# Kernel tuning notes

Hardware: AMD Instinct MI355X
Metric: run time of the kernel (lower is better)

## Reference

```python
import jax, jax.numpy as jnp
from jax import lax
import numpy as np

N, F_IN, D_MODEL = 8192, 128, 256
D_INNER, D_STATE, D_CONV, DT_RANK = 512, 16, 4, 16  # expand=2, d_state=16, d_conv=4, dt_rank=ceil(256/16)
BN_EPS = 1e-5


def setup_inputs() -> dict:
    key = jax.random.key(0)
    ks = jax.random.split(key, 12)
    rn = lambda k, s, sc: jax.random.normal(k, s, jnp.float32) * sc
    x = rn(ks[0], (N, F_IN), 1.0)
    # normalized dense adjacency (row sums ~1)
    adj = jax.random.uniform(ks[1], (N, N), jnp.float32) * (2.0 / N)
    w_gcn = rn(ks[2], (F_IN, D_MODEL), 1.0 / np.sqrt(F_IN))
    b_gcn = rn(ks[3], (D_MODEL,), 0.02)
    bn_gamma = jnp.ones((D_MODEL,), jnp.float32)
    bn_beta = jnp.zeros((D_MODEL,), jnp.float32)
    w_in = rn(ks[4], (2 * D_INNER, D_MODEL), 1.0 / np.sqrt(D_MODEL))
    conv_w = rn(ks[5], (D_INNER, D_CONV), 1.0 / np.sqrt(D_CONV))
    conv_b = rn(ks[6], (D_INNER,), 0.02)
    w_xproj = rn(ks[7], (DT_RANK + 2 * D_STATE, D_INNER), 1.0 / np.sqrt(D_INNER))
    w_dt = rn(ks[8], (D_INNER, DT_RANK), 1.0 / np.sqrt(DT_RANK))
    b_dt = rn(ks[9], (D_INNER,), 0.1)
    A_log = jnp.log(jnp.broadcast_to(jnp.arange(1, D_STATE + 1, dtype=jnp.float32), (D_INNER, D_STATE)))
    D_skip = jnp.ones((D_INNER,), jnp.float32)
    w_out = rn(ks[10], (D_MODEL, D_INNER), 1.0 / np.sqrt(D_INNER))
    return dict(x=x, adj=adj, w_gcn=w_gcn, b_gcn=b_gcn, bn_gamma=bn_gamma, bn_beta=bn_beta,
                w_in=w_in, conv_w=conv_w, conv_b=conv_b, w_xproj=w_xproj, w_dt=w_dt,
                b_dt=b_dt, A_log=A_log, D_skip=D_skip, w_out=w_out)


def _forward(x, adj, w_gcn, b_gcn, bn_gamma, bn_beta, w_in, conv_w, conv_b,
             w_xproj, w_dt, b_dt, A_log, D_skip, w_out):
    # --- GCN layer: adj @ (x @ W) + b ---
    h = adj @ (x @ w_gcn) + b_gcn            # (N, D_MODEL)
    h = jax.nn.relu(h)
    # dropout: eval mode -> identity
    # --- BatchNorm1d (batch statistics, biased var, as torch training norm) ---
    mean = jnp.mean(h, axis=0)
    var = jnp.var(h, axis=0)
    h = (h - mean) * lax.rsqrt(var + BN_EPS) * bn_gamma + bn_beta  # (N, D_MODEL)

    # --- Mamba block, batch=1, seq_len=N ---
    xz = h @ w_in.T                          # (N, 2*D_INNER)
    xm, z = jnp.split(xz, 2, axis=-1)        # (N, D_INNER) each

    # causal depthwise conv1d (kernel D_CONV) + SiLU
    xp = jnp.pad(xm, ((D_CONV - 1, 0), (0, 0)))
    xc = conv_b + sum(xp[i:i + N] * conv_w[:, i] for i in range(D_CONV))  # (N, D_INNER)
    xc = jax.nn.silu(xc)

    # input-dependent SSM parameters
    x_dbl = xc @ w_xproj.T                   # (N, DT_RANK + 2*D_STATE)
    dt_r = x_dbl[:, :DT_RANK]
    B = x_dbl[:, DT_RANK:DT_RANK + D_STATE]  # (N, D_STATE)
    C = x_dbl[:, DT_RANK + D_STATE:]         # (N, D_STATE)
    dt = jax.nn.softplus(dt_r @ w_dt.T + b_dt)  # (N, D_INNER)

    A = -jnp.exp(A_log)                      # (D_INNER, D_STATE)
    deltaA = jnp.exp(dt[:, :, None] * A[None])                 # (N, D_INNER, D_STATE)
    deltaBu = dt[:, :, None] * B[:, None, :] * xc[:, :, None]  # (N, D_INNER, D_STATE)

    def step(hs, inp):
        dA, dBu, c = inp
        hs = dA * hs + dBu                   # (D_INNER, D_STATE)
        return hs, hs @ c                    # emit (D_INNER,)

    h0 = jnp.zeros((D_INNER, D_STATE), xc.dtype)
    _, ys = lax.scan(step, h0, (deltaA, deltaBu, C))  # ys: (N, D_INNER)

    y = ys + D_skip * xc
    y = y * jax.nn.silu(z)
    out_m = y @ w_out.T                      # (N, D_MODEL)
    return out_m + h                         # residual


def reference(x, adj, w_gcn, b_gcn, bn_gamma, bn_beta, w_in, conv_w, conv_b,
              w_xproj, w_dt, b_dt, A_log, D_skip, w_out):
    return _forward(x, adj, w_gcn, b_gcn, bn_gamma, bn_beta, w_in, conv_w, conv_b,
                    w_xproj, w_dt, b_dt, A_log, D_skip, w_out)
```

## Files before the change

### kernel.cpp

```cpp
#include <hip/hip_runtime.h>
#include <stdint.h>

#define NN   8192
#define FIN  128
#define DM   256
#define DI   512
#define DST  16
#define NC   256
#define CL   32

typedef short bf16x8 __attribute__((ext_vector_type(8)));
typedef float f32x4 __attribute__((ext_vector_type(4)));
union FragU { unsigned u[4]; uint4 u4; bf16x8 v; };

__device__ __forceinline__ unsigned short f2bf(float x){
  unsigned u = __float_as_uint(x);
  return (unsigned short)((u + 0x7FFFu + ((u >> 16) & 1u)) >> 16);
}
__device__ __forceinline__ unsigned pack2(float a, float b){
  return (unsigned)f2bf(a) | ((unsigned)f2bf(b) << 16);
}
__device__ __forceinline__ unsigned pack2rn(float a, float b){
  unsigned ua = __float_as_uint(a) + 0x8000u;
  unsigned ub = __float_as_uint(b) + 0x8000u;
  return __builtin_amdgcn_perm(ub, ua, 0x07060302u);
}
__device__ __forceinline__ float bf2f(unsigned short u){
  return __uint_as_float(((unsigned)u) << 16);
}
__device__ __forceinline__ float sigmoidf_(float x){ return 1.f / (1.f + __expf(-x)); }
__device__ __forceinline__ f32x4 zero4(){ f32x4 z; z[0]=0.f; z[1]=0.f; z[2]=0.f; z[3]=0.f; return z; }

#define ASYNC16(g, l) __builtin_amdgcn_global_load_lds( \
    (const __attribute__((address_space(1))) void*)(g), \
    (__attribute__((address_space(3))) void*)(l), 16, 0, 0)
#define WAITVM8  asm volatile("s_waitcnt vmcnt(8)" ::: "memory")
#define WAITVM4  asm volatile("s_waitcnt vmcnt(4)" ::: "memory")
#define WAITVM3  asm volatile("s_waitcnt vmcnt(3)" ::: "memory")
#define WAITVM0  asm volatile("s_waitcnt vmcnt(0)" ::: "memory")
#define WAITLGKM0 asm volatile("s_waitcnt lgkmcnt(0)" ::: "memory")
#define BARRIER  asm volatile("s_barrier" ::: "memory")

constexpr size_t OFF_XWT   = 0;
constexpr size_t OFF_HB    = OFF_XWT   + (size_t)DM*NN*2;
constexpr size_t OFF_HBNB  = OFF_HB    + (size_t)NN*DM*2;
constexpr size_t OFF_WINB  = OFF_HBNB  + (size_t)NN*DM*2;
constexpr size_t OFF_WXPB  = OFF_WINB  + (size_t)1024*256*2;
constexpr size_t OFF_WOUTB = OFF_WXPB  + (size_t)48*512*2;
constexpr size_t OFF_XMB   = OFF_WOUTB + (size_t)256*512*2;
constexpr size_t OFF_ZB    = OFF_XMB   + (size_t)NN*DI*2;
constexpr size_t OFF_XC    = OFF_ZB    + (size_t)NN*DI*2;
constexpr size_t OFF_XCB   = OFF_XC    + (size_t)NN*DI*4;
constexpr size_t OFF_XDBL  = OFF_XCB   + (size_t)NN*DI*2;
constexpr size_t OFF_DT    = OFF_XDBL  + (size_t)NN*48*4;
constexpr size_t OFF_PF    = OFF_DT    + (size_t)NN*DI*4;
constexpr size_t OFF_CY    = OFF_PF    + (size_t)NC*DI*DST*8;
constexpr size_t OFF_YB    = OFF_CY    + (size_t)NC*DI*DST*4;
constexpr size_t OFF_BNS   = OFF_YB    + (size_t)NN*DI*2;
constexpr size_t OFF_BNS2  = OFF_BNS   + 256*4;
constexpr size_t WS_NEED   = OFF_BNS2  + 256*4;
constexpr size_t OFF_HP    = OFF_PF;

__global__ __launch_bounds__(256) void prep_kernel(
    const float* __restrict__ w_in, const float* __restrict__ w_xp, const float* __restrict__ w_out,
    unsigned short* __restrict__ o_in, unsigned short* __restrict__ o_xp, unsigned short* __restrict__ o_out)
{
  int i = blockIdx.x * 256 + threadIdx.x;
  if (i < 1024*256) o_in[i]  = f2bf(w_in[i]);
  if (i < 48*512)   o_xp[i]  = f2bf(w_xp[i]);
  if (i < 256*512)  o_out[i] = f2bf(w_out[i]);
}

__global__ __launch_bounds__(256) void gemm1_kernel(
    const float* __restrict__ x, const float* __restrict__ w, unsigned short* __restrict__ xwT)
{
  __shared__ float xs[16*128];
  const int t = threadIdx.x;
  const int m0 = blockIdx.x * 16;
  {
    int r = t >> 4, c0 = (t & 15) * 8;
    const float* src = x + (size_t)(m0 + r)*FIN + c0;
    *(float4*)&xs[r*128 + c0]     = *(const float4*)src;
    *(float4*)&xs[r*128 + c0 + 4] = *(const float4*)(src + 4);
  }
  __syncthreads();
  const int n = t;
  float acc[16];
  #pragma unroll
  for (int m = 0; m < 16; ++m) acc[m] = 0.f;
  for (int k = 0; k < 128; k += 4){
    float w0 = w[(size_t)k*DM + n];
    float w1 = w[(size_t)(k+1)*DM + n];
    float w2 = w[(size_t)(k+2)*DM + n];
    float w3 = w[(size_t)(k+3)*DM + n];
    #pragma unroll
    for (int m = 0; m < 16; ++m){
      float4 xv = *(const float4*)&xs[m*128 + k];
      acc[m] = fmaf(xv.x, w0, acc[m]);
      acc[m] = fmaf(xv.y, w1, acc[m]);
      acc[m] = fmaf(xv.z, w2, acc[m]);
      acc[m] = fmaf(xv.w, w3, acc[m]);
    }
  }
  unsigned outp[8];
  #pragma unroll
  for (int m = 0; m < 8; ++m) outp[m] = pack2(acc[2*m], acc[2*m+1]);
  unsigned short* dst = xwT + (size_t)n*NN + m0;
  ((uint4*)dst)[0] = *(uint4*)&outp[0];
  ((uint4*)dst)[1] = *(uint4*)&outp[4];
}

__global__ __launch_bounds__(512, 1) void gemm2_kernel(
    const float* __restrict__ adj, const unsigned short* __restrict__ xwT,
    float* __restrict__ hp)
{
  extern __shared__ char lds[];
  const int t = threadIdx.x;
  const int wave = t >> 6, lane = t & 63, r = lane & 15, q = lane >> 4;
  const int mt = (int)blockIdx.x >> 2, ks = (int)blockIdx.x & 3;
  const int m0 = mt * 128;
  const int kb = ks * 2048;
  const int wm = wave & 1, wn = wave >> 1;

  const int arow = t >> 3, ag = t & 7;
  const float* asrcA = adj + (size_t)(m0 + arow)*NN + kb + ((ag ^ (arow & 7)) << 2);
  const float* asrcB = asrcA + (size_t)64*NN;
  const int bnl = t >> 2, bg = t & 3;
  const unsigned short* bsrcA = xwT + (size_t)bnl*NN + kb + ((bg ^ ((bnl >> 1) & 3)) << 3);
  const unsigned short* bsrcB = bsrcA + (size_t)128*NN;
  const int dA0 = t*16, dA1 = 8192 + t*16, dB0 = 16384 + t*16, dB1 = 24576 + t*16;

  f32x4 acc[4][4];
  #pragma unroll
  for (int mi = 0; mi < 4; ++mi)
    #pragma unroll
    for (int ni = 0; ni < 4; ++ni) acc[mi][ni] = zero4();

  #pragma unroll
  for (int s = 0; s < 3; ++s){
    char* L = lds + s*32768;
    ASYNC16(asrcA + s*32, L + dA0);
    ASYNC16(asrcB + s*32, L + dA1);
    ASYNC16(bsrcA + s*32, L + dB0);
    ASYNC16(bsrcB + s*32, L + dB1);
  }

  int aoff[4][2], boff[4];
  #pragma unroll
  for (int mi = 0; mi < 4; ++mi){
    int row = wm*64 + mi*16 + r;
    aoff[mi][0] = row*32 + (((2*q)   ^ (row & 7)) << 2);
    aoff[mi][1] = row*32 + (((2*q+1) ^ (row & 7)) << 2);
  }
  #pragma unroll
  for (int ni = 0; ni < 4; ++ni){
    int nl = wn*64 + ni*16 + r;
    boff[ni] = nl*4 + (q ^ ((nl >> 1) & 3));
  }

  int rb = 0;
  for (int k = 0; k < 64; ++k){
    if (k < 62) { WAITVM8; } else if (k == 62) { WAITVM4; } else { WAITVM0; }
    BARRIER;
    char* Lb = lds + rb*32768;
    const float* Af = (const float*)Lb;
    const uint4* Bf = (const uint4*)(Lb + 16384);
    float4 pa[4][2];
    FragU fb[4];
    #pragma unroll
    for (int mi = 0; mi < 4; ++mi){
      pa[mi][0] = *(const float4*)(Af + aoff[mi][0]);
      pa[mi][1] = *(const float4*)(Af + aoff[mi][1]);
    }
    #pragma unroll
    for (int ni = 0; ni < 4; ++ni) fb[ni].u4 = Bf[boff[ni]];
    WAITLGKM0;
    BARRIER;
    if (k < 61){
      int ko = (k + 3) * 32;
      ASYNC16(asrcA + ko, Lb + dA0);
      ASYNC16(asrcB + ko, Lb + dA1);
      ASYNC16(bsrcA + ko, Lb + dB0);
      ASYNC16(bsrcB + ko, Lb + dB1);
    }
    FragU fa[4];
    #pragma unroll
    for (int mi = 0; mi < 4; ++mi){
      fa[mi].u[0] = pack2rn(pa[mi][0].x, pa[mi][0].y);
      fa[mi].u[1] = pack2rn(pa[mi][0].z, pa[mi][0].w);
      fa[mi].u[2] = pack2rn(pa[mi][1].x, pa[mi][1].y);
      fa[mi].u[3] = pack2rn(pa[mi][1].z, pa[mi][1].w);
    }
    #pragma unroll
    for (int mi = 0; mi < 4; ++mi)
      #pragma unroll
      for (int ni = 0; ni < 4; ++ni)
        acc[mi][ni] = __builtin_amdgcn_mfma_f32_16x16x32_bf16(fa[mi].v, fb[ni].v, acc[mi][ni], 0, 0, 0);
    rb = (rb == 2) ? 0 : rb + 1;
  }

  float* hpo = hp + (size_t)ks * ((size_t)NN * DM);
  #pragma unroll
  for (int mi = 0; mi < 4; ++mi)
    #pragma unroll
    for (int ni = 0; ni < 4; ++ni){
      const int n = wn*64 + ni*16 + r;
      #pragma unroll
      for (int jr = 0; jr < 4; ++jr){
        const int m = m0 + wm*64 + mi*16 + q*4 + jr;
        hpo[(size_t)m*DM + n] = acc[mi][ni][jr];
      }
    }
}

__global__ __launch_bounds__(256) void hred_kernel(
    const float* __restrict__ hp, const float* __restrict__ b_gcn,
    unsigned short* __restrict__ hb, float* __restrict__ bns, float* __restrict__ bns2)
{
  const size_t NND = (size_t)NN * DM;
  const int c = threadIdx.x;
  const int m0 = blockIdx.x * 32;
  const float bias = b_gcn[c];
  float s1 = 0.f, s2 = 0.f;
  #pragma unroll 8
  for (int rr = 0; rr < 32; ++rr){
    size_t idx = (size_t)(m0 + rr)*DM + c;
    float v = hp[idx] + hp[NND + idx] + hp[2*NND + idx] + hp[3*NND + idx] + bias;
    v = fmaxf(v, 0.f);
    hb[idx] = f2bf(v);
    s1 += v; s2 += v*v;
  }
  atomicAdd(bns + c, s1);
  atomicAdd(bns2 + c, s2);
}

__global__ __launch_bounds__(256) void bnapply_kernel(
    const unsigned short* __restrict__ hb, const float* __restrict__ s1, const float* __restrict__ s2,
    const float* __restrict__ gamma, const float* __restrict__ beta,
    unsigned short* __restrict__ hbnb)
{
  int base = (blockIdx.x*256 + threadIdx.x) * 2;
  int c0 = base & (DM - 1);
  ushort2 hv = *(const ushort2*)(hb + base);
  float mA = s1[c0] * (1.f/NN),   mB = s1[c0+1] * (1.f/NN);
  float vA = s2[c0] * (1.f/NN) - mA*mA, vB = s2[c0+1] * (1.f/NN) - mB*mB;
  float iA = rsqrtf(vA + 1e-5f), iB = rsqrtf(vB + 1e-5f);
  float a = (bf2f(hv.x) - mA)*iA*gamma[c0]   + beta[c0];
  float b = (bf2f(hv.y) - mB)*iB*gamma[c0+1] + beta[c0+1];
  ushort2 o; o.x = f2bf(a); o.y = f2bf(b);
  *(ushort2*)(hbnb + base) = o;
}

__global__ __launch_bounds__(256) void gemm3_kernel(
    const unsigned short* __restrict__ Ab, const unsigned short* __restrict__ Wb,
    unsigned short* __restrict__ xmb, unsigned short* __restrict__ zb)
{
  __shared__ uint4 alds[2048];
  const int t = threadIdx.x;
  const int wave = t >> 6, lane = t & 63, r = lane & 15, q = lane >> 4;
  const int mb = ((int)blockIdx.x & 127) * 64;
  const int nb = ((int)blockIdx.x >> 7) * 128;
  const int wm = wave & 1, wn = wave >> 1;

  #pragma unroll
  for (int j = 0; j < 8; ++j){
    int si = j*256 + t;
    int row = si >> 5, dg = si & 31;
    int sg = dg ^ (row & 31);
    ASYNC16(Ab + (size_t)(mb + row)*DM + sg*8, (char*)alds + si*16);
  }
  __syncthreads();

  f32x4 acc[2][4];
  #pragma unroll
  for (int mi = 0; mi < 2; ++mi)
    #pragma unroll
    for (int ni = 0; ni < 4; ++ni) acc[mi][ni] = zero4();

  const unsigned short* bp[4];
  #pragma unroll
  for (int ni = 0; ni < 4; ++ni)
    bp[ni] = Wb + (size_t)(nb + wn*64 + ni*16 + r)*DM + q*8;
  FragU fb[4];
  #pragma unroll
  for (int ni = 0; ni < 4; ++ni) fb[ni].u4 = *(const uint4*)bp[ni];

  #pragma unroll
  for (int it = 0; it < 8; ++it){
    FragU fbn[4];
    if (it < 7){
      #pragma unroll
      for (int ni = 0; ni < 4; ++ni) fbn[ni].u4 = *(const uint4*)(bp[ni] + (it+1)*32);
    }
    FragU fa[2];
    #pragma unroll
    for (int mi = 0; mi < 2; ++mi){
      int row = wm*32 + mi*16 + r;
      int g = it*4 + q;
      fa[mi].u4 = alds[row*32 + (g ^ (row & 31))];
    }
    #pragma unroll
    for (int mi = 0; mi < 2; ++mi)
      #pragma unroll
      for (int ni = 0; ni < 4; ++ni)
        acc[mi][ni] = __builtin_amdgcn_mfma_f32_16x16x32_bf16(fa[mi].v, fb[ni].v, acc[mi][ni], 0, 0, 0);
    if (it < 7){
      #pragma unroll
      for (int ni = 0; ni < 4; ++ni) fb[ni] = fbn[ni];
    }
  }
  #pragma unroll
  for (int mi = 0; mi < 2; ++mi)
    #pragma unroll
    for (int ni = 0; ni < 4; ++ni){
      int nc = nb + wn*64 + ni*16 + r;
      unsigned short* dst = (nc < 512) ? (xmb + nc) : (zb + (nc - 512));
      #pragma unroll
      for (int jr = 0; jr < 4; ++jr){
        int m = mb + wm*32 + mi*16 + q*4 + jr;
        dst[(size_t)m*DI] = f2bf(acc[mi][ni][jr]);
      }
    }
}

__global__ __launch_bounds__(256) void conv_kernel(
    const unsigned short* __restrict__ xmb, const float* __restrict__ conv_w, const float* __restrict__ conv_b,
    float* __restrict__ xc, unsigned short* __restrict__ xcb)
{
  const int d0 = threadIdx.x * 2;
  const int n0 = blockIdx.x * 32;
  float4 wa = *(const float4*)(conv_w + (size_t)d0*4);
  float4 wb = *(const float4*)(conv_w + (size_t)d0*4 + 4);
  float2 bias = *(const float2*)(conv_b + d0);
  float x0a=0.f,x1a=0.f,x2a=0.f, x0b=0.f,x1b=0.f,x2b=0.f;
  #pragma unroll
  for (int j = 0; j < 3; ++j){
    int n = n0 - 3 + j;
    float va = 0.f, vb = 0.f;
    if (n >= 0){
      ushort2 u = *(const ushort2*)(xmb + (size_t)n*DI + d0);
      va = bf2f(u.x); vb = bf2f(u.y);
    }
    if (j == 0){ x0a = va; x0b = vb; }
    else if (j == 1){ x1a = va; x1b = vb; }
    else { x2a = va; x2b = vb; }
  }
  for (int j = 0; j < 32; ++j){
    int n = n0 + j;
    ushort2 u = *(const ushort2*)(xmb + (size_t)n*DI + d0);
    float x3a = bf2f(u.x), x3b = bf2f(u.y);
    float sa = bias.x + wa.x*x0a + wa.y*x1a + wa.z*x2a + wa.w*x3a;
    float sb = bias.y + wb.x*x0b + wb.y*x1b + wb.z*x2b + wb.w*x3b;
    float va = sa * sigmoidf_(sa);
    float vb = sb * sigmoidf_(sb);
    *(float2*)(xc + (size_t)n*DI + d0) = make_float2(va, vb);
    ushort2 o; o.x = f2bf(va); o.y = f2bf(vb);
    *(ushort2*)(xcb + (size_t)n*DI + d0) = o;
    x0a=x1a; x1a=x2a; x2a=x3a;
    x0b=x1b; x1b=x2b; x2b=x3b;
  }
}

__global__ __launch_bounds__(256) void gemm4_kernel(
    const unsigned short* __restrict__ Ab, const unsigned short* __restrict__ Wb, float* __restrict__ xdbl)
{
  __shared__ uint4 alds[2048];
  const int t = threadIdx.x;
  const int wave = t >> 6, lane = t & 63, r = lane & 15, q = lane >> 4;
  const int m0 = (int)blockIdx.x * 32;
  #pragma unroll
  for (int j = 0; j < 8; ++j){
    int si = j*256 + t;
    int row = si >> 6, dg = si & 63;
    int sg = dg ^ (row & 31);
    ASYNC16(Ab + (size_t)(m0 + row)*DI + sg*8, (char*)alds + si*16);
  }
  __syncthreads();
  f32x4 acc[2][3];
  #pragma unroll
  for (int mi = 0; mi < 2; ++mi)
    #pragma unroll
    for (int ni = 0; ni < 3; ++ni) acc[mi][ni] = zero4();
  const int kq = wave * 128;
  const unsigned short* bp[3];
  #pragma unroll
  for (int ni = 0; ni < 3; ++ni) bp[ni] = Wb + (size_t)(ni*16 + r)*DI + kq + q*8;
  FragU fb[3];
  #pragma unroll
  for (int ni = 0; ni < 3; ++ni) fb[ni].u4 = *(const uint4*)bp[ni];
  #pragma unroll
  for (int it = 0; it < 4; ++it){
    FragU fbn[3];
    if (it < 3){
      #pragma unroll
      for (int ni = 0; ni < 3; ++ni) fbn[ni].u4 = *(const uint4*)(bp[ni] + (it+1)*32);
    }
    FragU fa[2];
    #pragma unroll
    for (int mi = 0; mi < 2; ++mi){
      int row = mi*16 + r;
      int g = (kq >> 3) + it*4 + q;
      fa[mi].u4 = alds[row*64 + (g ^ (row & 31))];
    }
    #pragma unroll
    for (int mi = 0; mi < 2; ++mi)
      #pragma unroll
      for (int ni = 0; ni < 3; ++ni)
        acc[mi][ni] = __builtin_amdgcn_mfma_f32_16x16x32_bf16(fa[mi].v, fb[ni].v, acc[mi][ni], 0, 0, 0);
    if (it < 3){
      #pragma unroll
      for (int ni = 0; ni < 3; ++ni) fb[ni] = fbn[ni];
    }
  }
  __syncthreads();
  float* red = (float*)alds;
  if (wave > 0){
    int base = ((wave - 1)*64 + lane)*24;
    #pragma unroll
    for (int mi = 0; mi < 2; ++mi)
      #pragma unroll
      for (int ni = 0; ni < 3; ++ni)
        #pragma unroll
        for (int jr = 0; jr < 4; ++jr)
          red[base + (mi*3 + ni)*4 + jr] = acc[mi][ni][jr];
  }
  __syncthreads();
  if (wave == 0){
    #pragma unroll
    for (int w = 0; w < 3; ++w){
      int base = (w*64 + lane)*24;
      #pragma unroll
      for (int mi = 0; mi < 2; ++mi)
        #pragma unroll
        for (int ni = 0; ni < 3; ++ni)
          #pragma unroll
          for (int jr = 0; jr < 4; ++jr)
            acc[mi][ni][jr] += red[base + (mi*3 + ni)*4 + jr];
    }
    #pragma unroll
    for (int mi = 0; mi < 2; ++mi)
      #pragma unroll
      for (int ni = 0; ni < 3; ++ni)
        #pragma unroll
        for (int jr = 0; jr < 4; ++jr)
          xdbl[(size_t)(m0 + mi*16 + q*4 + jr)*48 + ni*16 + r] = acc[mi][ni][jr];
  }
}

__global__ __launch_bounds__(256) void dt_kernel(
    const float* __restrict__ xdbl, const float* __restrict__ w_dt, const float* __restrict__ b_dt,
    float* __restrict__ dt)
{
  __shared__ float xr[64*16];
  const int t = threadIdx.x;
  const int dg = (int)blockIdx.x & 1;
  const int n0 = ((int)blockIdx.x >> 1) * 64;
  const int d = dg*256 + t;
  #pragma unroll
  for (int j = 0; j < 4; ++j){
    int idx = t + 256*j;
    xr[idx] = xdbl[(size_t)(n0 + (idx >> 4))*48 + (idx & 15)];
  }
  __syncthreads();
  const float4* wp = (const float4*)(w_dt + (size_t)d*16);
  float4 w0 = wp[0], w1 = wp[1], w2 = wp[2], w3 = wp[3];
  float bias = b_dt[d];
  for (int j = 0; j < 64; ++j){
    const float4* xp = (const float4*)(xr + j*16);
    float4 a0 = xp[0], a1 = xp[1], a2 = xp[2], a3 = xp[3];
    float a = bias;
    a += w0.x*a0.x + w0.y*a0.y + w0.z*a0.z + w0.w*a0.w;
    a += w1.x*a1.x + w1.y*a1.y + w1.z*a1.z + w1.w*a1.w;
    a += w2.x*a2.x + w2.y*a2.y + w2.z*a2.z + w2.w*a2.w;
    a += w3.x*a3.x + w3.y*a3.y + w3.z*a3.z + w3.w*a3.w;
    float o = (a > 20.f) ? a : log1pf(__expf(a));
    dt[(size_t)(n0 + j)*DI + d] = o;
  }
}

__global__ __launch_bounds__(256) void scanA_kernel(
    const float* __restrict__ dt, const float* __restrict__ xc,
    const float* __restrict__ xdbl, const float* __restrict__ A_log,
    float2* __restrict__ PF)
{
  __shared__ float Bs[CL*DST];
  const int t = threadIdx.x;
  const int c = (int)blockIdx.x >> 1;
  const int d = (((int)blockIdx.x & 1) << 8) + t;
  #pragma unroll
  for (int j = 0; j < 2; ++j){
    int idx = t + 256*j;
    Bs[idx] = xdbl[(size_t)(c*CL + (idx >> 4))*48 + 16 + (idx & 15)];
  }
  __syncthreads();
  float Av[DST], hs[DST];
  {
    const float4* Ap = (const float4*)(A_log + (size_t)d*DST);
    #pragma unroll
    for (int s4 = 0; s4 < 4; ++s4){
      float4 a4 = Ap[s4];
      Av[s4*4+0] = -__expf(a4.x); Av[s4*4+1] = -__expf(a4.y);
      Av[s4*4+2] = -__expf(a4.z); Av[s4*4+3] = -__expf(a4.w);
    }
  }
  #pragma unroll
  for (int s = 0; s < DST; ++s) hs[s] = 0.f;
  float sdt = 0.f;
  const size_t rb = (size_t)c*CL*DI + d;
  float dtv = dt[rb], xcv = xc[rb];
  for (int tt = 0; tt < CL; ++tt){
    float dtn = 0.f, xcn = 0.f;
    if (tt + 1 < CL){
      dtn = dt[rb + (size_t)(tt+1)*DI];
      xcn = xc[rb + (size_t)(tt+1)*DI];
    }
    float u = dtv * xcv;
    sdt += dtv;
    float bv[DST];
    *(float4*)&bv[0]  = *(const float4*)&Bs[tt*16];
    *(float4*)&bv[4]  = *(const float4*)&Bs[tt*16 + 4];
    *(float4*)&bv[8]  = *(const float4*)&Bs[tt*16 + 8];
    *(float4*)&bv[12] = *(const float4*)&Bs[tt*16 + 12];
    #pragma unroll
    for (int s = 0; s < DST; ++s)
      hs[s] = __expf(dtv * Av[s]) * hs[s] + u * bv[s];
    dtv = dtn; xcv = xcn;
  }
  float4* out = (float4*)(PF + (size_t)c*(DI*DST) + (size_t)d*DST);
  #pragma unroll
  for (int j = 0; j < 8; ++j){
    float4 v;
    v.x = __expf(Av[2*j] * sdt);   v.y = hs[2*j];
    v.z = __expf(Av[2*j+1] * sdt); v.w = hs[2*j+1];
    out[j] = v;
  }
}

__global__ __launch_bounds__(128) void scanB_kernel(
    const float2* __restrict__ PF, float* __restrict__ Cy)
{
  const int ds = (int)blockIdx.x*128 + (int)threadIdx.x;
  float2 A0[16], A1[16];
  #pragma unroll
  for (int j = 0; j < 16; ++j) A0[j] = PF[(size_t)j*8192 + ds];
  #pragma unroll
  for (int j = 0; j < 16; ++j) A1[j] = PF[(size_t)(16 + j)*8192 + ds];
  float cy = 0.f;
  Cy[ds] = 0.f;
  #pragma unroll
  for (int g = 0; g < 16; ++g){
    #pragma unroll
    for (int j = 0; j < 16; ++j){
      int i = g*16 + j;
      if (i < NC - 1){
        float2 pf = (g & 1) ? A1[j] : A0[j];
        cy = pf.x * cy + pf.y;
        Cy[(size_t)(i + 1)*8192 + ds] = cy;
      }
    }
    int gn = g + 2;
    if (gn < 16){
      #pragma unroll
      for (int j = 0; j < 16; ++j){
        float2 v = PF[(size_t)(gn*16 + j)*8192 + ds];
        if (g & 1) A1[j] = v; else A0[j] = v;
      }
    }
  }
}

__global__ __launch_bounds__(256) void scanC_kernel(
    const float* __restrict__ dt, const float* __restrict__ xc,
    const float* __restrict__ xdbl, const float* __restrict__ A_log,
    const float* __restrict__ Cy, const float* __restrict__ Dskip,
    const unsigned short* __restrict__ zb, unsigned short* __restrict__ yb)
{
  __shared__ float Bs[CL*DST];
  __shared__ float Cs[CL*DST];
  const int t = threadIdx.x;
  const int c = (int)blockIdx.x >> 1;
  const int d = (((int)blockIdx.x & 1) << 8) + t;
  #pragma unroll
  for (int j = 0; j < 2; ++j){
    int idx = t + 256*j;
    int tg = c*CL + (idx >> 4);
    Bs[idx] = xdbl[(size_t)tg*48 + 16 + (idx & 15)];
    Cs[idx] = xdbl[(size_t)tg*48 + 32 + (idx & 15)];
  }
  __syncthreads();
  float Av[DST], hs[DST];
  {
    const float4* Ap = (const float4*)(A_log + (size_t)d*DST);
    #pragma unroll
    for (int s4 = 0; s4 < 4; ++s4){
      float4 a4 = Ap[s4];
      Av[s4*4+0] = -__expf(a4.x); Av[s4*4+1] = -__expf(a4.y);
      Av[s4*4+2] = -__expf(a4.z); Av[s4*4+3] = -__expf(a4.w);
    }
  }
  {
    const float4* hp4 = (const float4*)(Cy + (size_t)c*(DI*DST) + (size_t)d*DST);
    #pragma unroll
    for (int s4 = 0; s4 < 4; ++s4){
      float4 h4 = hp4[s4];
      hs[s4*4+0] = h4.x; hs[s4*4+1] = h4.y; hs[s4*4+2] = h4.z; hs[s4*4+3] = h4.w;
    }
  }
  const float Dv = Dskip[d];
  const size_t rb = (size_t)c*CL*DI + d;
  float dtv = dt[rb], xcv = xc[rb];
  unsigned short zv0 = zb[rb];
  for (int tt = 0; tt < CL; ++tt){
    float dtn = 0.f, xcn = 0.f;
    unsigned short zn = 0;
    if (tt + 1 < CL){
      dtn = dt[rb + (size_t)(tt+1)*DI];
      xcn = xc[rb + (size_t)(tt+1)*DI];
      zn  = zb[rb + (size_t)(tt+1)*DI];
    }
    float u = dtv * xcv;
    float bv[DST], cv[DST];
    *(float4*)&bv[0]  = *(const float4*)&Bs[tt*16];
    *(float4*)&bv[4]  = *(const float4*)&Bs[tt*16 + 4];
    *(float4*)&bv[8]  = *(const float4*)&Bs[tt*16 + 8];
    *(float4*)&bv[12] = *(const float4*)&Bs[tt*16 + 12];
    *(float4*)&cv[0]  = *(const float4*)&Cs[tt*16];
    *(float4*)&cv[4]  = *(const float4*)&Cs[tt*16 + 4];
    *(float4*)&cv[8]  = *(const float4*)&Cs[tt*16 + 8];
    *(float4*)&cv[12] = *(const float4*)&Cs[tt*16 + 12];
    float y0 = 0.f, y1 = 0.f;
    #pragma unroll
    for (int s = 0; s < DST; s += 2){
      hs[s]   = __expf(dtv * Av[s])   * hs[s]   + u * bv[s];
      hs[s+1] = __expf(dtv * Av[s+1]) * hs[s+1] + u * bv[s+1];
      y0 += hs[s]   * cv[s];
      y1 += hs[s+1] * cv[s+1];
    }
    float z = bf2f(zv0);
    float yf = ((y0 + y1) + Dv * xcv) * (z * sigmoidf_(z));
    yb[rb + (size_t)tt*DI] = f2bf(yf);
    dtv = dtn; xcv = xcn; zv0 = zn;
  }
}

__global__ __launch_bounds__(512) void gemm5_kernel(
    const unsigned short* __restrict__ yb, const unsigned short* __restrict__ Wb,
    const unsigned short* __restrict__ hbnb, float* __restrict__ out)
{
  __shared__ uint4 alds[2048];
  const int t = threadIdx.x;
  const int wave = t >> 6, lane = t & 63, r = lane & 15, q = lane >> 4;
  const int m0 = (int)blockIdx.x * 32;
  #pragma unroll
  for (int j = 0; j < 4; ++j){
    int si = j*512 + t;
    int row = si >> 6, dg = si & 63;
    int sg = dg ^ (row & 31);
    ASYNC16(yb + (size_t)(m0 + row)*DI + sg*8, (char*)alds + si*16);
  }
  __syncthreads();
  f32x4 acc[2][2];
  #pragma unroll
  for (int mi = 0; mi < 2; ++mi)
    #pragma unroll
    for (int ni = 0; ni < 2; ++ni) acc[mi][ni] = zero4();
  const int nw = wave * 32;
  const unsigned short* bp0 = Wb + (size_t)(nw + r)*DI + q*8;
  const unsigned short* bp1 = Wb + (size_t)(nw + 16 + r)*DI + q*8;
  FragU fb0, fb1;
  fb0.u4 = *(const uint4*)bp0;
  fb1.u4 = *(const uint4*)bp1;
  #pragma unroll
  for (int it = 0; it < 16; ++it){
    FragU fn0, fn1;
    if (it < 15){
      fn0.u4 = *(const uint4*)(bp0 + (it+1)*32);
      fn1.u4 = *(const uint4*)(bp1 + (it+1)*32);
    }
    FragU fa[2];
    #pragma unroll
    for (int mi = 0; mi < 2; ++mi){
      int row = mi*16 + r;
      int g = it*4 + q;
      fa[mi].u4 = alds[row*64 + (g ^ (row & 31))];
    }
    acc[0][0] = __builtin_amdgcn_mfma_f32_16x16x32_bf16(fa[0].v, fb0.v, acc[0][0], 0, 0, 0);
    acc[0][1] = __builtin_amdgcn_mfma_f32_16x16x32_bf16(fa[0].v, fb1.v, acc[0][1], 0, 0, 0);
    acc[1][0] = __builtin_amdgcn_mfma_f32_16x16x32_bf16(fa[1].v, fb0.v, acc[1][0], 0, 0, 0);
    acc[1][1] = __builtin_amdgcn_mfma_f32_16x16x32_bf16(fa[1].v, fb1.v, acc[1][1], 0, 0, 0);
    if (it < 15){ fb0 = fn0; fb1 = fn1; }
  }
  #pragma unroll
  for (int mi = 0; mi < 2; ++mi)
    #pragma unroll
    for (int ni = 0; ni < 2; ++ni){
      const int n = nw + ni*16 + r;
      #pragma unroll
      for (int jr = 0; jr < 4; ++jr){
        const int m = m0 + mi*16 + q*4 + jr;
        size_t idx = (size_t)m*DM + n;
        out[idx] = acc[mi][ni][jr] + bf2f(hbnb[idx]);
      }
    }
}

extern "C" void kernel_launch(void* const* d_in, const int* in_sizes, int n_in,
                              void* d_out, int out_size, void* d_ws, size_t ws_size,
                              hipStream_t stream)
{
  const float* x      = (const float*)d_in[0];
  const float* adj    = (const float*)d_in[1];
  const float* w_gcn  = (const float*)d_in[2];
  const float* b_gcn  = (const float*)d_in[3];
  const float* gamma  = (const float*)d_in[4];
  const float* beta   = (const float*)d_in[5];
  const float* w_in   = (const float*)d_in[6];
  const float* conv_w = (const float*)d_in[7];
  const float* conv_b = (const float*)d_in[8];
  const float* w_xp   = (const float*)d_in[9];
  const float* w_dt   = (const float*)d_in[10];
  const float* b_dt   = (const float*)d_in[11];
  const float* A_log  = (const float*)d_in[12];
  const float* D_skip = (const float*)d_in[13];
  const float* w_out  = (const float*)d_in[14];
  float* out = (float*)d_out;
  char* ws = (char*)d_ws;
  if (ws_size < WS_NEED) return;

  unsigned short* xwT   = (unsigned short*)(ws + OFF_XWT);
  float*          hp    = (float*)(ws + OFF_HP);
  unsigned short* hb    = (unsigned short*)(ws + OFF_HB);
  unsigned short* hbnb  = (unsigned short*)(ws + OFF_HBNB);
  unsigned short* winb  = (unsigned short*)(ws + OFF_WINB);
  unsigned short* wxpb  = (unsigned short*)(ws + OFF_WXPB);
  unsigned short* woutb = (unsigned short*)(ws + OFF_WOUTB);
  unsigned short* xmb   = (unsigned short*)(ws + OFF_XMB);
  unsigned short* zb    = (unsigned short*)(ws + OFF_ZB);
  float*          xc    = (float*)(ws + OFF_XC);
  unsigned short* xcb   = (unsigned short*)(ws + OFF_XCB);
  float*          xdbl  = (float*)(ws + OFF_XDBL);
  float*          dtb   = (float*)(ws + OFF_DT);
  float2*         PF    = (float2*)(ws + OFF_PF);
  float*          Cy    = (float*)(ws + OFF_CY);
  unsigned short* yb    = (unsigned short*)(ws + OFF_YB);
  float*          bns   = (float*)(ws + OFF_BNS);
  float*          bns2  = (float*)(ws + OFF_BNS2);

  hipMemsetAsync(bns, 0, 2*256*sizeof(float), stream);

  hipFuncSetAttribute((const void*)gemm2_kernel,
                      hipFuncAttributeMaxDynamicSharedMemorySize, 98304);

  prep_kernel   <<<1024, 256, 0, stream>>>(w_in, w_xp, w_out, winb, wxpb, woutb);
  gemm1_kernel  <<<512,  256, 0, stream>>>(x, w_gcn, xwT);
  gemm2_kernel  <<<256,  512, 98304, stream>>>(adj, xwT, hp);
  hred_kernel   <<<256,  256, 0, stream>>>(hp, b_gcn, hb, bns, bns2);
  bnapply_kernel<<<4096, 256, 0, stream>>>(hb, bns, bns2, gamma, beta, hbnb);
  gemm3_kernel  <<<1024, 256, 0, stream>>>(hbnb, winb, xmb, zb);
  conv_kernel   <<<256,  256, 0, stream>>>(xmb, conv_w, conv_b, xc, xcb);
  gemm4_kernel  <<<256,  256, 0, stream>>>(xcb, wxpb, xdbl);
  dt_kernel     <<<256,  256, 0, stream>>>(xdbl, w_dt, b_dt, dtb);
  scanA_kernel  <<<512,  256, 0, stream>>>(dtb, xc, xdbl, A_log, PF);
  scanB_kernel  <<<64,   128, 0, stream>>>(PF, Cy);
  scanC_kernel  <<<512,  256, 0, stream>>>(dtb, xc, xdbl, A_log, Cy, D_skip, zb, yb);
  gemm5_kernel  <<<256,  512, 0, stream>>>(yb, woutb, hbnb, out);
}
```

Baseline: 598.0 us.

## Retile adjacency GEMM into 32-row blocks and drop fp32 conv output buffer

The adj@XW GEMM is retiled from 128-row tiles with 512 threads to 32-row tiles with 256 threads and 1024 blocks. It uses a double-buffered 64-wide K step with a rotation swizzle and allows two blocks per CU, aiming for more parallelism on the bandwidth-bound 256MB adjacency read. Separately, the fp32 xc buffer is removed and the scan kernels read the bf16 copy instead, cutting memory traffic at the cost of lower precision in the scan inputs. The smaller M tile means each XW tile is reloaded four times as often, which adds B-side traffic.

```diff
diff --git a/kernel.cpp b/kernel.cpp
--- a/kernel.cpp
+++ b/kernel.cpp
@@ -34,9 +34,7 @@
 #define ASYNC16(g, l) __builtin_amdgcn_global_load_lds( \
     (const __attribute__((address_space(1))) void*)(g), \
     (__attribute__((address_space(3))) void*)(l), 16, 0, 0)
-#define WAITVM8  asm volatile("s_waitcnt vmcnt(8)" ::: "memory")
-#define WAITVM4  asm volatile("s_waitcnt vmcnt(4)" ::: "memory")
-#define WAITVM3  asm volatile("s_waitcnt vmcnt(3)" ::: "memory")
+#define WAITVM10 asm volatile("s_waitcnt vmcnt(10)" ::: "memory")
 #define WAITVM0  asm volatile("s_waitcnt vmcnt(0)" ::: "memory")
 #define WAITLGKM0 asm volatile("s_waitcnt lgkmcnt(0)" ::: "memory")
 #define BARRIER  asm volatile("s_barrier" ::: "memory")
@@ -49,8 +47,7 @@
 constexpr size_t OFF_WOUTB = OFF_WXPB  + (size_t)48*512*2;
 constexpr size_t OFF_XMB   = OFF_WOUTB + (size_t)256*512*2;
 constexpr size_t OFF_ZB    = OFF_XMB   + (size_t)NN*DI*2;
-constexpr size_t OFF_XC    = OFF_ZB    + (size_t)NN*DI*2;
-constexpr size_t OFF_XCB   = OFF_XC    + (size_t)NN*DI*4;
+constexpr size_t OFF_XCB   = OFF_ZB    + (size_t)NN*DI*2;
 constexpr size_t OFF_XDBL  = OFF_XCB   + (size_t)NN*DI*2;
 constexpr size_t OFF_DT    = OFF_XDBL  + (size_t)NN*48*4;
 constexpr size_t OFF_PF    = OFF_DT    + (size_t)NN*DI*4;
@@ -110,7 +107,7 @@
   ((uint4*)dst)[1] = *(uint4*)&outp[4];
 }
 
-__global__ __launch_bounds__(512, 1) void gemm2_kernel(
+__global__ __launch_bounds__(256, 2) void gemm2_kernel(
     const float* __restrict__ adj, const unsigned short* __restrict__ xwT,
     float* __restrict__ hp)
 {
@@ -118,96 +115,118 @@
   const int t = threadIdx.x;
   const int wave = t >> 6, lane = t & 63, r = lane & 15, q = lane >> 4;
   const int mt = (int)blockIdx.x >> 2, ks = (int)blockIdx.x & 3;
-  const int m0 = mt * 128;
+  const int m0 = mt * 32;
   const int kb = ks * 2048;
-  const int wm = wave & 1, wn = wave >> 1;
-
-  const int arow = t >> 3, ag = t & 7;
-  const float* asrcA = adj + (size_t)(m0 + arow)*NN + kb + ((ag ^ (arow & 7)) << 2);
-  const float* asrcB = asrcA + (size_t)64*NN;
-  const int bnl = t >> 2, bg = t & 3;
-  const unsigned short* bsrcA = xwT + (size_t)bnl*NN + kb + ((bg ^ ((bnl >> 1) & 3)) << 3);
-  const unsigned short* bsrcB = bsrcA + (size_t)128*NN;
-  const int dA0 = t*16, dA1 = 8192 + t*16, dB0 = 16384 + t*16, dB1 = 24576 + t*16;
-
-  f32x4 acc[4][4];
-  #pragma unroll
-  for (int mi = 0; mi < 4; ++mi)
+
+  const float* asrc[2];
+  #pragma unroll
+  for (int j = 0; j < 2; ++j){
+    int si = t + 256*j;
+    int row = si >> 4, d = si & 15;
+    int g = (d - 3*row) & 15;
+    asrc[j] = adj + (size_t)(m0 + row)*NN + kb + g*4;
+  }
+  const unsigned short* bsrc[8];
+  #pragma unroll
+  for (int j = 0; j < 8; ++j){
+    int si = t + 256*j;
+    int n = si >> 3, d = si & 7;
+    int g = (d - 3*n) & 7;
+    bsrc[j] = xwT + (size_t)n*NN + kb + g*8;
+  }
+
+  f32x4 acc[2][4];
+  #pragma unroll
+  for (int mi = 0; mi < 2; ++mi)
     #pragma unroll
     for (int ni = 0; ni < 4; ++ni) acc[mi][ni] = zero4();
 
   #pragma unroll
-  for (int s = 0; s < 3; ++s){
-    char* L = lds + s*32768;
-    ASYNC16(asrcA + s*32, L + dA0);
-    ASYNC16(asrcB + s*32, L + dA1);
-    ASYNC16(bsrcA + s*32, L + dB0);
-    ASYNC16(bsrcB + s*32, L + dB1);
-  }
-
-  int aoff[4][2], boff[4];
-  #pragma unroll
-  for (int mi = 0; mi < 4; ++mi){
-    int row = wm*64 + mi*16 + r;
-    aoff[mi][0] = row*32 + (((2*q)   ^ (row & 7)) << 2);
-    aoff[mi][1] = row*32 + (((2*q+1) ^ (row & 7)) << 2);
-  }
-  #pragma unroll
-  for (int ni = 0; ni < 4; ++ni){
-    int nl = wn*64 + ni*16 + r;
-    boff[ni] = nl*4 + (q ^ ((nl >> 1) & 3));
-  }
-
-  int rb = 0;
-  for (int k = 0; k < 64; ++k){
-    if (k < 62) { WAITVM8; } else if (k == 62) { WAITVM4; } else { WAITVM0; }
+  for (int s = 0; s < 2; ++s){
+    char* L = lds + s*40960;
+    int k0 = s*64;
+    ASYNC16(asrc[0] + k0, L + t*16);
+    ASYNC16(asrc[1] + k0, L + (t + 256)*16);
+    #pragma unroll
+    for (int j = 0; j < 8; ++j)
+      ASYNC16(bsrc[j] + k0, L + 8192 + (t + 256*j)*16);
+  }
+
+  int aoffF[2][2][2];
+  int boffU[2][4];
+  #pragma unroll
+  for (int ks2 = 0; ks2 < 2; ++ks2){
+    #pragma unroll
+    for (int mi = 0; mi < 2; ++mi){
+      int m = mi*16 + r;
+      int g0 = ks2*8 + 2*q;
+      aoffF[ks2][mi][0] = m*64 + (((g0    ) + 3*m) & 15)*4;
+      aoffF[ks2][mi][1] = m*64 + (((g0 + 1) + 3*m) & 15)*4;
+    }
+    #pragma unroll
+    for (int ni = 0; ni < 4; ++ni){
+      int n = wave*64 + ni*16 + r;
+      int g = ks2*4 + q;
+      boffU[ks2][ni] = 512 + n*8 + ((g + 3*n) & 7);
+    }
+  }
+
+  for (int k = 0; k < 32; ++k){
+    if (k < 31) { WAITVM10; } else { WAITVM0; }
     BARRIER;
-    char* Lb = lds + rb*32768;
+    char* Lb = lds + (k & 1)*40960;
     const float* Af = (const float*)Lb;
-    const uint4* Bf = (const uint4*)(Lb + 16384);
-    float4 pa[4][2];
-    FragU fb[4];
-    #pragma unroll
-    for (int mi = 0; mi < 4; ++mi){
-      pa[mi][0] = *(const float4*)(Af + aoff[mi][0]);
-      pa[mi][1] = *(const float4*)(Af + aoff[mi][1]);
-    }
-    #pragma unroll
-    for (int ni = 0; ni < 4; ++ni) fb[ni].u4 = Bf[boff[ni]];
+    const uint4* Bu = (const uint4*)Lb;
+    float4 pa[2][2][2];
+    FragU fb[2][4];
+    #pragma unroll
+    for (int ks2 = 0; ks2 < 2; ++ks2){
+      #pragma unroll
+      for (int mi = 0; mi < 2; ++mi){
+        pa[ks2][mi][0] = *(const float4*)(Af + aoffF[ks2][mi][0]);
+        pa[ks2][mi][1] = *(const float4*)(Af + aoffF[ks2][mi][1]);
+      }
+      #pragma unroll
+      for (int ni = 0; ni < 4; ++ni) fb[ks2][ni].u4 = Bu[boffU[ks2][ni]];
+    }
     WAITLGKM0;
     BARRIER;
-    if (k < 61){
-      int ko = (k + 3) * 32;
-      ASYNC16(asrcA + ko, Lb + dA0);
-      ASYNC16(asrcB + ko, Lb + dA1);
-      ASYNC16(bsrcA + ko, Lb + dB0);
-      ASYNC16(bsrcB + ko, Lb + dB1);
-    }
-    FragU fa[4];
-    #pragma unroll
-    for (int mi = 0; mi < 4; ++mi){
-      fa[mi].u[0] = pack2rn(pa[mi][0].x, pa[mi][0].y);
-      fa[mi].u[1] = pack2rn(pa[mi][0].z, pa[mi][0].w);
-      fa[mi].u[2] = pack2rn(pa[mi][1].x, pa[mi][1].y);
-      fa[mi].u[3] = pack2rn(pa[mi][1].z, pa[mi][1].w);
-    }
-    #pragma unroll
-    for (int mi = 0; mi < 4; ++mi)
-      #pragma unroll
-      for (int ni = 0; ni < 4; ++ni)
-        acc[mi][ni] = __builtin_amdgcn_mfma_f32_16x16x32_bf16(fa[mi].v, fb[ni].v, acc[mi][ni], 0, 0, 0);
-    rb = (rb == 2) ? 0 : rb + 1;
+    if (k < 30){
+      int k0 = (k + 2) * 64;
+      ASYNC16(asrc[0] + k0, Lb + t*16);
+      ASYNC16(asrc[1] + k0, Lb + (t + 256)*16);
+      #pragma unroll
+      for (int j = 0; j < 8; ++j)
+        ASYNC16(bsrc[j] + k0, Lb + 8192 + (t + 256*j)*16);
+    }
+    FragU fa[2][2];
+    #pragma unroll
+    for (int ks2 = 0; ks2 < 2; ++ks2)
+      #pragma unroll
+      for (int mi = 0; mi < 2; ++mi){
+        fa[ks2][mi].u[0] = pack2rn(pa[ks2][mi][0].x, pa[ks2][mi][0].y);
+        fa[ks2][mi].u[1] = pack2rn(pa[ks2][mi][0].z, pa[ks2][mi][0].w);
+        fa[ks2][mi].u[2] = pack2rn(pa[ks2][mi][1].x, pa[ks2][mi][1].y);
+        fa[ks2][mi].u[3] = pack2rn(pa[ks2][mi][1].z, pa[ks2][mi][1].w);
+      }
+    #pragma unroll
+    for (int ks2 = 0; ks2 < 2; ++ks2)
+      #pragma unroll
+      for (int mi = 0; mi < 2; ++mi)
+        #pragma unroll
+        for (int ni = 0; ni < 4; ++ni)
+          acc[mi][ni] = __builtin_amdgcn_mfma_f32_16x16x32_bf16(fa[ks2][mi].v, fb[ks2][ni].v, acc[mi][ni], 0, 0, 0);
   }
 
   float* hpo = hp + (size_t)ks * ((size_t)NN * DM);
   #pragma unroll
-  for (int mi = 0; mi < 4; ++mi)
+  for (int mi = 0; mi < 2; ++mi)
     #pragma unroll
     for (int ni = 0; ni < 4; ++ni){
-      const int n = wn*64 + ni*16 + r;
+      const int n = wave*64 + ni*16 + r;
       #pragma unroll
       for (int jr = 0; jr < 4; ++jr){
-        const int m = m0 + wm*64 + mi*16 + q*4 + jr;
+        const int m = m0 + mi*16 + q*4 + jr;
         hpo[(size_t)m*DM + n] = acc[mi][ni][jr];
       }
     }
@@ -325,7 +344,7 @@
 
 __global__ __launch_bounds__(256) void conv_kernel(
     const unsigned short* __restrict__ xmb, const float* __restrict__ conv_w, const float* __restrict__ conv_b,
-    float* __restrict__ xc, unsigned short* __restrict__ xcb)
+    unsigned short* __restrict__ xcb)
 {
   const int d0 = threadIdx.x * 2;
   const int n0 = blockIdx.x * 32;
@@ -353,7 +372,6 @@
     float sb = bias.y + wb.x*x0b + wb.y*x1b + wb.z*x2b + wb.w*x3b;
     float va = sa * sigmoidf_(sa);
     float vb = sb * sigmoidf_(sb);
-    *(float2*)(xc + (size_t)n*DI + d0) = make_float2(va, vb);
     ushort2 o; o.x = f2bf(va); o.y = f2bf(vb);
     *(ushort2*)(xcb + (size_t)n*DI + d0) = o;
     x0a=x1a; x1a=x2a; x2a=x3a;
@@ -443,7 +461,7 @@
       for (int ni = 0; ni < 3; ++ni)
         #pragma unroll
         for (int jr = 0; jr < 4; ++jr)
-          xdbl[(size_t)(m0 + mi*16 + q*4 + jr)*48 + ni*16 + r] = acc[mi][ni][jr];
+          xdbl[(size_t)(m0 + mi*16 + q*4 + jr)*48 + ni*16 + r] = acc[ni >= 0 ? mi : mi][ni][jr];
   }
 }
 
@@ -479,7 +497,7 @@
 }
 
 __global__ __launch_bounds__(256) void scanA_kernel(
-    const float* __restrict__ dt, const float* __restrict__ xc,
+    const float* __restrict__ dt, const unsigned short* __restrict__ xcb,
     const float* __restrict__ xdbl, const float* __restrict__ A_log,
     float2* __restrict__ PF)
 {
@@ -507,12 +525,12 @@
   for (int s = 0; s < DST; ++s) hs[s] = 0.f;
   float sdt = 0.f;
   const size_t rb = (size_t)c*CL*DI + d;
-  float dtv = dt[rb], xcv = xc[rb];
+  float dtv = dt[rb], xcv = bf2f(xcb[rb]);
   for (int tt = 0; tt < CL; ++tt){
     float dtn = 0.f, xcn = 0.f;
     if (tt + 1 < CL){
       dtn = dt[rb + (size_t)(tt+1)*DI];
-      xcn = xc[rb + (size_t)(tt+1)*DI];
+      xcn = bf2f(xcb[rb + (size_t)(tt+1)*DI]);
     }
     float u = dtv * xcv;
     sdt += dtv;
@@ -570,7 +588,7 @@
 }
 
 __global__ __launch_bounds__(256) void scanC_kernel(
-    const float* __restrict__ dt, const float* __restrict__ xc,
+    const float* __restrict__ dt, const unsigned short* __restrict__ xcb,
     const float* __restrict__ xdbl, const float* __restrict__ A_log,
     const float* __restrict__ Cy, const float* __restrict__ Dskip,
     const unsigned short* __restrict__ zb, unsigned short* __restrict__ yb)
@@ -608,14 +626,14 @@
   }
   const float Dv = Dskip[d];
   const size_t rb = (size_t)c*CL*DI + d;
-  float dtv = dt[rb], xcv = xc[rb];
+  float dtv = dt[rb], xcv = bf2f(xcb[rb]);
   unsigned short zv0 = zb[rb];
   for (int tt = 0; tt < CL; ++tt){
     float dtn = 0.f, xcn = 0.f;
     unsigned short zn = 0;
     if (tt + 1 < CL){
       dtn = dt[rb + (size_t)(tt+1)*DI];
-      xcn = xc[rb + (size_t)(tt+1)*DI];
+      xcn = bf2f(xcb[rb + (size_t)(tt+1)*DI]);
       zn  = zb[rb + (size_t)(tt+1)*DI];
     }
     float u = dtv * xcv;
@@ -736,7 +754,6 @@
   unsigned short* woutb = (unsigned short*)(ws + OFF_WOUTB);
   unsigned short* xmb   = (unsigned short*)(ws + OFF_XMB);
   unsigned short* zb    = (unsigned short*)(ws + OFF_ZB);
-  float*          xc    = (float*)(ws + OFF_XC);
   unsigned short* xcb   = (unsigned short*)(ws + OFF_XCB);
   float*          xdbl  = (float*)(ws + OFF_XDBL);
   float*          dtb   = (float*)(ws + OFF_DT);
@@ -749,19 +766,19 @@
   hipMemsetAsync(bns, 0, 2*256*sizeof(float), stream);
 
   hipFuncSetAttribute((const void*)gemm2_kernel,
-                      hipFuncAttributeMaxDynamicSharedMemorySize, 98304);
+                      hipFuncAttributeMaxDynamicSharedMemorySize, 81920);
 
   prep_kernel   <<<1024, 256, 0, stream>>>(w_in, w_xp, w_out, winb, wxpb, woutb);
   gemm1_kernel  <<<512,  256, 0, stream>>>(x, w_gcn, xwT);
-  gemm2_kernel  <<<256,  512, 98304, stream>>>(adj, xwT, hp);
+  gemm2_kernel  <<<1024, 256, 81920, stream>>>(adj, xwT, hp);
   hred_kernel   <<<256,  256, 0, stream>>>(hp, b_gcn, hb, bns, bns2);
   bnapply_kernel<<<4096, 256, 0, stream>>>(hb, bns, bns2, gamma, beta, hbnb);
   gemm3_kernel  <<<1024, 256, 0, stream>>>(hbnb, winb, xmb, zb);
-  conv_kernel   <<<256,  256, 0, stream>>>(xmb, conv_w, conv_b, xc, xcb);
+  conv_kernel   <<<256,  256, 0, stream>>>(xmb, conv_w, conv_b, xcb);
   gemm4_kernel  <<<256,  256, 0, stream>>>(xcb, wxpb, xdbl);
   dt_kernel     <<<256,  256, 0, stream>>>(xdbl, w_dt, b_dt, dtb);
-  scanA_kernel  <<<512,  256, 0, stream>>>(dtb, xc, xdbl, A_log, PF);
+  scanA_kernel  <<<512,  256, 0, stream>>>(dtb, xcb, xdbl, A_log, PF);
   scanB_kernel  <<<64,   128, 0, stream>>>(PF, Cy);
-  scanC_kernel  <<<512,  256, 0, stream>>>(dtb, xc, xdbl, A_log, Cy, D_skip, zb, yb);
+  scanC_kernel  <<<512,  256, 0, stream>>>(dtb, xcb, xdbl, A_log, Cy, D_skip, zb, yb);
   gemm5_kernel  <<<256,  512, 0, stream>>>(yb, woutb, hbnb, out);
 }
```

After: 601.9 us. About the same (+0.6%).
